# Performance work log

Hardware: AMD Instinct MI355X
Metric: run time of the kernel (lower is better)

The kernel has to match this reference:

```python
import jax, jax.numpy as jnp
import numpy as np

N_TAU = 100  # number of steps per delay interval: dt = tau / N_TAU = 0.01 * tau


def _F(x, y, t, params):
    # Delay-logistic vector field: x'(t) = theta0 * x(t) * (1 - theta1 * x(t - tau))
    return params[0] * x * (1.0 - params[1] * y)


def setup_inputs() -> dict:
    key = jax.random.key(0)
    k1, = jax.random.split(key, 1)
    d = 32768
    x_0 = jax.random.uniform(k1, (d,), dtype=jnp.float32)  # positive ICs, stable dynamics
    tau = jnp.ones((1,), dtype=jnp.float32)
    params = jnp.ones((2,), dtype=jnp.float32)  # theta0, theta1
    N = 1000  # T = N * dt = 10 * tau
    return {"x_0": x_0, "tau": tau, "params": params, "N": N}


def reference(x_0, tau, params, N):
    # Forward-Euler DDE solve with constant history x(t) = x_0 for t in [-tau, 0].
    d = x_0.shape[0]
    dt = 0.01 * tau[0]
    dtype = x_0.dtype
    traj0 = jnp.zeros((N + 1, d), dtype=dtype).at[0].set(x_0)  # rows are time steps

    def step(traj, i):
        x_i = traj[i]                                            # current state [d]
        # delayed state x(t_i - tau): history (= x_0) for the first N_TAU steps
        y_i = jnp.where(i >= N_TAU, traj[jnp.maximum(i - N_TAU, 0)], x_0)
        t_i = i.astype(dtype) * dt
        x_next = x_i + dt * _F(x_i, y_i, t_i, params)
        return traj.at[i + 1].set(x_next), None

    traj, _ = jax.lax.scan(step, traj0, jnp.arange(N))
    # match torch convention: kth COLUMN is the state at the kth time step -> [d, N+1]
    return traj.T
```

## Files before the change

### kernel.cpp

```cpp
#include <hip/hip_runtime.h>


constexpr int NT   = 1000;
constexpr int NTAU = 100;
constexpr int NPH  = 5;
constexpr int PCOL = 200;
constexpr int NP1  = NT + 1;
constexpr int COMP = 64;
constexpr int LSTR = PCOL + 1;
constexpr int NCW  = 3;

#define R5(F,B)   F(B) F((B)+1) F((B)+2) F((B)+3) F((B)+4)
#define R25(F,B)  R5(F,B) R5(F,(B)+5) R5(F,(B)+10) R5(F,(B)+15) R5(F,(B)+20)
#define R50(F,B)  R25(F,B) R25(F,(B)+25)
#define R100(F)   R50(F,0) R50(F,50)

#define LDS_ORDER() do {                                    \
    __builtin_amdgcn_sched_barrier(0);                      \
    asm volatile("s_waitcnt lgkmcnt(0)" ::: "memory");      \
    __builtin_amdgcn_sched_barrier(0);                      \
} while (0)

__global__ __launch_bounds__(256, 1)
void ndde_kernel(const float* __restrict__ x0,
                 const float* __restrict__ tau,
                 const float* __restrict__ params,
                 float* __restrict__ out)
{
    __shared__ float buf[2][COMP][LSTR];
    __shared__ int   prodf;
    __shared__ int   consf[NCW];
    const int tid  = threadIdx.x;
    const int wid  = tid >> 6;
    const int lane = tid & 63;
    const int jbase = (int)blockIdx.x * COMP;

    const float dt = 0.01f * tau[0];
    const float a  = dt * params[0];
    const float q  = -(a * params[1]);
    const float p  = 1.0f + a;

    if (tid == 0) { prodf = 0; consf[0] = 0; consf[1] = 0; consf[2] = 0; }
    __syncthreads();

    volatile int* vprod = &prodf;
    volatile int* vcons = consf;

    if (wid == 0) {
        float x = x0[jbase + lane];
        float h[NTAU];
#define INIT_H(K) h[(K)] = x;
        R100(INIT_H)
#define STEP(K) { const float y_ = h[(K)]; h[(K)] = x; x *= fmaf(q, y_, p); }
#define STG0(K) bp[(K)] = h[(K)];
#define STG1(K) bp[100+(K)] = h[(K)];

#pragma clang loop unroll(disable)
        for (int ph = 0; ph < NPH; ++ph) {
            if (ph >= 2) {
                while (vcons[0] < ph - 1 || vcons[1] < ph - 1 || vcons[2] < ph - 1)
                    __builtin_amdgcn_s_sleep(1);
                LDS_ORDER();
            }
            float* bp = &buf[ph & 1][lane][0];
            R100(STEP)
            R100(STG0)
            R100(STEP)
            R100(STG1)
            LDS_ORDER();
            *vprod = ph + 1;
        }
        out[(jbase + lane) * NP1 + NT] = x;
    } else {
        const int cw    = wid - 1;
        const int start = (cw == 0) ? 0 : (cw == 1) ? 22 : 43;
        const int cnt   = (cw == 0) ? 22 : 21;
        const int lane8 = (lane < 8) ? lane : 7;
        float* gpb = out + (jbase + start) * NP1 + lane;

#pragma clang loop unroll(disable)
        for (int ph = 0; ph < NPH; ++ph) {
            while (*vprod < ph + 1)
                __builtin_amdgcn_s_sleep(1);
            LDS_ORDER();
            const float* bb = &buf[ph & 1][start][0];
            float* gp = gpb + ph * PCOL;

            for (int r = 0; r < cnt; r += 2) {
                const int r1 = (r + 1 < cnt) ? r + 1 : r;
                const float* la = bb + r  * LSTR;
                const float* lb = bb + r1 * LSTR;
                float a0 = la[lane], a1 = la[64 + lane], a2 = la[128 + lane];
                float a3 = la[192 + lane8];
                float b0 = lb[lane], b1 = lb[64 + lane], b2 = lb[128 + lane];
                float b3 = lb[192 + lane8];
                float* ra = gp + r  * NP1;
                float* rb = gp + r1 * NP1;
                ra[0] = a0; ra[64] = a1; ra[128] = a2;
                if (lane < 8) ra[192] = a3;
                if (r1 != r) {
                    rb[0] = b0; rb[64] = b1; rb[128] = b2;
                    if (lane < 8) rb[192] = b3;
                }
            }
            LDS_ORDER();
            vcons[cw] = ph + 1;
        }
    }
}

extern "C" void kernel_launch(void* const* d_in, const int* in_sizes, int n_in,
                              void* d_out, int out_size, void* d_ws, size_t ws_size,
                              hipStream_t stream) {
    const float* x0     = (const float*)d_in[0];
    const float* tau    = (const float*)d_in[1];
    const float* params = (const float*)d_in[2];
    float* out = (float*)d_out;
    const int d = in_sizes[0];
    const int nblocks = d / COMP;
    ndde_kernel<<<nblocks, 256, 0, stream>>>(x0, tau, params, out);
}
```

Baseline: 31.51 us.

## Write trajectory rows with aligned float4 stores using LDS prefix staging

Output rows have stride 1001 floats, so row starts are misaligned. The consumer waves now compute a per-row 16-byte-aligned offset and write each row with float4 stores. To cover the misaligned heads across phases, the producer stages an extra 32-column prefix from the previous phase, and the final state goes into LDS. This adds index arithmetic, a wider LDS row (stride 233) and head/tail scalar stores, in exchange for fewer and wider global store transactions.

```diff
diff --git a/kernel.cpp b/kernel.cpp
--- a/kernel.cpp
+++ b/kernel.cpp
@@ -7,11 +7,13 @@
 constexpr int PCOL = 200;
 constexpr int NP1  = NT + 1;
 constexpr int COMP = 64;
-constexpr int LSTR = PCOL + 1;
+constexpr int LSTR = 233;
 constexpr int NCW  = 3;
 
+#define R2(F,B)   F(B) F((B)+1)
 #define R5(F,B)   F(B) F((B)+1) F((B)+2) F((B)+3) F((B)+4)
 #define R25(F,B)  R5(F,B) R5(F,(B)+5) R5(F,(B)+10) R5(F,(B)+15) R5(F,(B)+20)
+#define R32(F,B)  R25(F,B) R5(F,(B)+25) R2(F,(B)+30)
 #define R50(F,B)  R25(F,B) R25(F,(B)+25)
 #define R100(F)   R50(F,0) R50(F,50)
 
@@ -52,8 +54,9 @@
 #define INIT_H(K) h[(K)] = x;
         R100(INIT_H)
 #define STEP(K) { const float y_ = h[(K)]; h[(K)] = x; x *= fmaf(q, y_, p); }
-#define STG0(K) bp[(K)] = h[(K)];
-#define STG1(K) bp[100+(K)] = h[(K)];
+#define PFX(K)  bp[(K)] = h[68+(K)];
+#define STG0(K) bp[32+(K)]  = h[(K)];
+#define STG1(K) bp[132+(K)] = h[(K)];
 
 #pragma clang loop unroll(disable)
         for (int ph = 0; ph < NPH; ++ph) {
@@ -63,44 +66,52 @@
                 LDS_ORDER();
             }
             float* bp = &buf[ph & 1][lane][0];
+            if (ph > 0) { R32(PFX, 0) }
             R100(STEP)
             R100(STG0)
             R100(STEP)
             R100(STG1)
+            if (ph == NPH - 1) bp[232] = x;
             LDS_ORDER();
             *vprod = ph + 1;
         }
-        out[(jbase + lane) * NP1 + NT] = x;
     } else {
-        const int cw    = wid - 1;
-        const int start = (cw == 0) ? 0 : (cw == 1) ? 22 : 43;
-        const int cnt   = (cw == 0) ? 22 : 21;
-        const int lane8 = (lane < 8) ? lane : 7;
-        float* gpb = out + (jbase + start) * NP1 + lane;
+        const int cw = wid - 1;
+        const int r0 = (cw == 0) ? 0 : (cw == 1) ? 22 : 43;
+        const int rn = (cw == 0) ? 22 : 21;
 
 #pragma clang loop unroll(disable)
         for (int ph = 0; ph < NPH; ++ph) {
             while (*vprod < ph + 1)
                 __builtin_amdgcn_s_sleep(1);
             LDS_ORDER();
-            const float* bb = &buf[ph & 1][start][0];
-            float* gp = gpb + ph * PCOL;
+            const int Lp = PCOL * ph;
+            const int Lc = (ph == NPH - 1) ? (NT + 1) : (Lp + PCOL);
 
-            for (int r = 0; r < cnt; r += 2) {
-                const int r1 = (r + 1 < cnt) ? r + 1 : r;
-                const float* la = bb + r  * LSTR;
-                const float* lb = bb + r1 * LSTR;
-                float a0 = la[lane], a1 = la[64 + lane], a2 = la[128 + lane];
-                float a3 = la[192 + lane8];
-                float b0 = lb[lane], b1 = lb[64 + lane], b2 = lb[128 + lane];
-                float b3 = lb[192 + lane8];
-                float* ra = gp + r  * NP1;
-                float* rb = gp + r1 * NP1;
-                ra[0] = a0; ra[64] = a1; ra[128] = a2;
-                if (lane < 8) ra[192] = a3;
-                if (r1 != r) {
-                    rb[0] = b0; rb[64] = b1; rb[128] = b2;
-                    if (lane < 8) rb[192] = b3;
+            for (int rr = 0; rr < rn; ++rr) {
+                const int r   = r0 + rr;
+                const int off = (32 - ((9 * r) & 31)) & 31;
+                const int cp  = (ph == 0) ? 0 : (Lp - off) >> 5;
+                const int cn  = (Lc - off) >> 5;
+                const int s   = off + (cp << 5);
+                const int nl  = (cn - cp) << 3;
+                const float* br = &buf[ph & 1][r][0];
+                float* rowp = out + (jbase + r) * NP1;
+
+                if (lane < nl) {
+                    const int col = s + 4 * lane;
+                    const int idx = col - Lp + 32;
+                    float4 v;
+                    v.x = br[idx]; v.y = br[idx + 1];
+                    v.z = br[idx + 2]; v.w = br[idx + 3];
+                    *(float4*)(rowp + col) = v;
+                }
+                if (ph == 0 && lane < off)
+                    rowp[lane] = br[32 + lane];
+                if (ph == NPH - 1) {
+                    const int t0 = off + (cn << 5);
+                    if (lane < (NT + 1) - t0)
+                        rowp[t0 + lane] = br[t0 + lane - Lp + 32];
                 }
             }
             LDS_ORDER();
```

After: 49.39 us. 56.7% more time.

## Vectorize global stores as aligned float4 with per-row alignment prefix/tail handling

Applied to the files above, without the earlier changes.

The producer wave now keeps the last four history values as a prefix in the LDS staging row. It also pads the LDS stride to 205 and stores the final state into the buffer. The consumer waves then issue 16-byte float4 LDS reads and global writes aligned to each output row's 4-element boundary, with scalar fixups for the row head and tail. This cuts the number of store instructions compared with the previous scalar 4-per-lane stores. In exchange it adds complex index arithmetic, possible misaligned LDS vector reads, and more LDS bank conflicts.

```diff
diff --git a/kernel.cpp b/kernel.cpp
--- a/kernel.cpp
+++ b/kernel.cpp
@@ -7,9 +7,10 @@
 constexpr int PCOL = 200;
 constexpr int NP1  = NT + 1;
 constexpr int COMP = 64;
-constexpr int LSTR = PCOL + 1;
+constexpr int LSTR = 205;
 constexpr int NCW  = 3;
 
+#define R4(F,B)   F(B) F((B)+1) F((B)+2) F((B)+3)
 #define R5(F,B)   F(B) F((B)+1) F((B)+2) F((B)+3) F((B)+4)
 #define R25(F,B)  R5(F,B) R5(F,(B)+5) R5(F,(B)+10) R5(F,(B)+15) R5(F,(B)+20)
 #define R50(F,B)  R25(F,B) R25(F,(B)+25)
@@ -52,8 +53,9 @@
 #define INIT_H(K) h[(K)] = x;
         R100(INIT_H)
 #define STEP(K) { const float y_ = h[(K)]; h[(K)] = x; x *= fmaf(q, y_, p); }
-#define STG0(K) bp[(K)] = h[(K)];
-#define STG1(K) bp[100+(K)] = h[(K)];
+#define PFX(K)  bp[(K)]     = h[96+(K)];
+#define STG0(K) bp[4+(K)]   = h[(K)];
+#define STG1(K) bp[104+(K)] = h[(K)];
 
 #pragma clang loop unroll(disable)
         for (int ph = 0; ph < NPH; ++ph) {
@@ -63,44 +65,64 @@
                 LDS_ORDER();
             }
             float* bp = &buf[ph & 1][lane][0];
+            if (ph > 0) { R4(PFX, 0) }
             R100(STEP)
             R100(STG0)
             R100(STEP)
             R100(STG1)
+            if (ph == NPH - 1) bp[204] = x;
             LDS_ORDER();
             *vprod = ph + 1;
         }
-        out[(jbase + lane) * NP1 + NT] = x;
     } else {
-        const int cw    = wid - 1;
-        const int start = (cw == 0) ? 0 : (cw == 1) ? 22 : 43;
-        const int cnt   = (cw == 0) ? 22 : 21;
-        const int lane8 = (lane < 8) ? lane : 7;
-        float* gpb = out + (jbase + start) * NP1 + lane;
+        const int cw = wid - 1;
+        const int r0 = (cw == 0) ? 0 : (cw == 1) ? 22 : 43;
+        const int rn = (cw == 0) ? 22 : 21;
 
 #pragma clang loop unroll(disable)
         for (int ph = 0; ph < NPH; ++ph) {
             while (*vprod < ph + 1)
                 __builtin_amdgcn_s_sleep(1);
             LDS_ORDER();
-            const float* bb = &buf[ph & 1][start][0];
-            float* gp = gpb + ph * PCOL;
+            const float* bb = &buf[ph & 1][0][0];
 
-            for (int r = 0; r < cnt; r += 2) {
-                const int r1 = (r + 1 < cnt) ? r + 1 : r;
-                const float* la = bb + r  * LSTR;
-                const float* lb = bb + r1 * LSTR;
-                float a0 = la[lane], a1 = la[64 + lane], a2 = la[128 + lane];
-                float a3 = la[192 + lane8];
-                float b0 = lb[lane], b1 = lb[64 + lane], b2 = lb[128 + lane];
-                float b3 = lb[192 + lane8];
-                float* ra = gp + r  * NP1;
-                float* rb = gp + r1 * NP1;
-                ra[0] = a0; ra[64] = a1; ra[128] = a2;
-                if (lane < 8) ra[192] = a3;
-                if (r1 != r) {
-                    rb[0] = b0; rb[64] = b1; rb[128] = b2;
-                    if (lane < 8) rb[192] = b3;
+            for (int rr = 0; rr < rn; rr += 2) {
+                const int  r1 = r0 + rr;
+                const bool two = (rr + 1 < rn);
+                const int  r2 = two ? (r1 + 1) : r1;
+
+                const int o1 = (-r1) & 3,  o2 = (-r2) & 3;
+                const int S1 = (ph == 0) ? o1 : (PCOL * ph + ((o1 - 1) & 3) - 3);
+                const int S2 = (ph == 0) ? o2 : (PCOL * ph + ((o2 - 1) & 3) - 3);
+                const int G1 = (ph == 0) ? ((o1 == 0) ? 50 : 49)
+                             : (ph == NPH - 1 && o1 == 1) ? 51 : 50;
+                const int G2 = (ph == 0) ? ((o2 == 0) ? 50 : 49)
+                             : (ph == NPH - 1 && o2 == 1) ? 51 : 50;
+
+                const float4* lp1 = (const float4*)(bb + r1 * LSTR + (S1 - PCOL * ph + 4));
+                const float4* lp2 = (const float4*)(bb + r2 * LSTR + (S2 - PCOL * ph + 4));
+                float* gp1 = out + (size_t)(jbase + r1) * NP1 + S1;
+                float* gp2 = out + (size_t)(jbase + r2) * NP1 + S2;
+
+                float4 v1, v2;
+                if (lane < G1) v1 = lp1[lane];
+                if (two && lane < G2) v2 = lp2[lane];
+                if (lane < G1) *(float4*)(gp1 + 4 * lane) = v1;
+                if (two && lane < G2) *(float4*)(gp2 + 4 * lane) = v2;
+
+                if (ph == 0) {
+                    if (lane < o1) gp1[lane - S1] = bb[r1 * LSTR + 4 + lane];
+                    if (two && lane < o2) gp2[lane - S2] = bb[r2 * LSTR + 4 + lane];
+                } else if (ph == NPH - 1) {
+                    const int t1 = (o1 == 0) ? 1 : (o1 == 1) ? 0 : (o1 == 2) ? 3 : 2;
+                    const int t2 = (o2 == 0) ? 1 : (o2 == 1) ? 0 : (o2 == 2) ? 3 : 2;
+                    const int c1 = NP1 - t1, c2 = NP1 - t2;
+                    if (lane < t1)
+                        out[(size_t)(jbase + r1) * NP1 + c1 + lane] =
+                            bb[r1 * LSTR + (c1 - 800 + 4) + lane];
+                    if (two && lane < t2)
+                        out[(size_t)(jbase + r2) * NP1 + c2 + lane] =
+                            bb[r2 * LSTR + (c2 - 800 + 4) + lane];
                 }
             }
             LDS_ORDER();
```

New measurement: 47.89 us. 1.52x slower.
